# Optimization experiments

Measured on AMD Instinct MI355X. Metric: run time of the kernel, lower is better.

## Reference

```python
import jax, jax.numpy as jnp
import numpy as np

M = 4
L_LIST = [5, 7, 9, 11]
C = 256
GC = C // M  # group channels = 64
BN_EPS = 1e-5


def setup_inputs() -> dict:
    key = jax.random.key(0)
    ks = jax.random.split(key, 12)
    B, H, W = 4, 128, 128
    x = jax.random.normal(ks[0], (B, C, H, W), dtype=jnp.float32)
    # per-group 1x1 conv weights (no bias), stacked since same shape
    qw = jax.random.normal(ks[1], (M, GC, GC), dtype=jnp.float32) * 0.05
    kw = jax.random.normal(ks[2], (M, GC, GC), dtype=jnp.float32) * 0.05
    r_q = jax.random.normal(ks[3], (1, C, 1, 1), dtype=jnp.float32)
    rk0 = jax.random.normal(ks[4], (1, GC, 2 * L_LIST[0] - 1, 1, 1), dtype=jnp.float32)
    rk1 = jax.random.normal(ks[5], (1, GC, 2 * L_LIST[1] - 1, 1, 1), dtype=jnp.float32)
    rk2 = jax.random.normal(ks[6], (1, GC, 2 * L_LIST[2] - 1, 1, 1), dtype=jnp.float32)
    rk3 = jax.random.normal(ks[7], (1, GC, 2 * L_LIST[3] - 1, 1, 1), dtype=jnp.float32)
    fusion_w = jax.random.normal(ks[8], (C, C), dtype=jnp.float32) * 0.05
    bn_gamma = jnp.ones((C,), dtype=jnp.float32)
    bn_beta = jnp.zeros((C,), dtype=jnp.float32)
    return {"x": x, "qw": qw, "kw": kw, "r_q": r_q, "rk0": rk0, "rk1": rk1,
            "rk2": rk2, "rk3": rk3, "fusion_w": fusion_w,
            "bn_gamma": bn_gamma, "bn_beta": bn_beta}


def _axial(k, L):
    """Gather the cross-shaped (axial) neighborhood of size 2L-1 per pixel.

    Matches F.unfold(k, (L,L), padding=pad) followed by slicing the center
    column (vertical neighbors) and center row minus the center element
    (horizontal neighbors), in the original ordering:
      [k_h (L vertical), k_w_pre (pad left), k_w_post (L-pad-1 right)].
    Returns [B, gc, 2L-1, H, W] with zero padding at borders.
    """
    pad = (L - 1) // 2
    B, gc, H, W = k.shape
    kv = jnp.pad(k, ((0, 0), (0, 0), (pad, pad), (0, 0)))
    kh = jnp.pad(k, ((0, 0), (0, 0), (0, 0), (pad, pad)))
    parts = [kv[:, :, r:r + H, :] for r in range(L)]            # vertical offsets -pad..pad
    parts += [kh[:, :, :, r:r + W] for r in range(pad)]          # horizontal -pad..-1
    parts += [kh[:, :, :, r:r + W] for r in range(pad + 1, L)]   # horizontal +1..+pad
    return jnp.stack(parts, axis=2)


def reference(x, qw, kw, r_q, rk0, rk1, rk2, rk3, fusion_w, bn_gamma, bn_beta):
    rks = [rk0, rk1, rk2, rk3]
    B, Cc, H, W = x.shape
    qx = r_q + x
    outs = []
    for i, L in enumerate(L_LIST):
        xg = x[:, i * GC:(i + 1) * GC]
        qg = qx[:, i * GC:(i + 1) * GC]
        q = jnp.einsum('oc,bchw->bohw', qw[i], qg)   # 1x1 conv, no bias
        k = jnp.einsum('oc,bchw->bohw', kw[i], xg)
        ka = _axial(k, L) + rks[i]                   # [B, gc, 2L-1, H, W]
        # energy over channels then summed over the 2L-1 axial positions
        e = jnp.einsum('bchw,bcrhw->bhw', q, ka)
        outs.append(jnp.broadcast_to(e[:, None], (B, GC, H, W)))
    att = jnp.concatenate(outs, axis=1)              # [B, C, H, W]
    att = jnp.einsum('oc,bchw->bohw', fusion_w, att)
    # BatchNorm2d in training mode: batch statistics over (B, H, W)
    mean = att.mean(axis=(0, 2, 3))
    var = att.var(axis=(0, 2, 3))
    att = (att - mean[:, None, None]) * jax.lax.rsqrt(var[:, None, None] + BN_EPS)
    att = att * bn_gamma[:, None, None] + bn_beta[:, None, None]
    att = jax.nn.sigmoid(jax.nn.relu(att))
    return x * att
```

## Files before the change

### kernel.cpp

```cpp
#include <hip/hip_runtime.h>

#define Bb 4
#define Cc 256
#define GC_ 64
#define Hh 128
#define Wd 128
#define HWn 16384
#define NPIX 65536
#define EPS 1e-5f

#define T_OFF   0
#define E_OFF   16777216
#define ST_OFF  (E_OFF + NPIX*4)
#define A_OFF   (ST_OFF + 16)
#define CV_OFF  (A_OFF + 16384)
#define FW_OFF  (CV_OFF + 256)

typedef __attribute__((ext_vector_type(8))) short short8v;
typedef __attribute__((ext_vector_type(4))) float f32x4;
typedef unsigned short u16;

__device__ inline u16 f2bf(float f) {
    union { float f; unsigned u; } v; v.f = f;
    unsigned r = v.u + 0x7fff + ((v.u >> 16) & 1);
    return (u16)(r >> 16);
}
__device__ inline float bf2f(u16 u) {
    union { unsigned u; float f; } v; v.u = ((unsigned)u) << 16;
    return v.f;
}

__global__ __launch_bounds__(256) void k0_precompute(
    const float* __restrict__ qw, const float* __restrict__ kw,
    const float* __restrict__ rk0, const float* __restrict__ rk1,
    const float* __restrict__ rk2, const float* __restrict__ rk3,
    const float* __restrict__ fusion_w,
    u16* __restrict__ Abf, float* __restrict__ cvec, float* __restrict__ fwred,
    float* __restrict__ stats)
{
    const int tid = threadIdx.x;
    if (blockIdx.x == 4) {
        if (tid < 16) stats[tid] = 0.f;
        for (int i = 0; i < 4; ++i) {
            float s = 0.f;
            const float* fp = fusion_w + tid*256 + i*64;
            #pragma unroll 8
            for (int c = 0; c < 64; ++c) s += fp[c];
            fwred[tid*4 + i] = s;
        }
        return;
    }
    const int g = blockIdx.x;
    __shared__ float qwL[4096];
    __shared__ float kwL[4096];
    __shared__ float rks[64];
    for (int i = tid; i < 4096; i += 256) {
        qwL[i] = qw[g*4096 + i];
        kwL[i] = kw[g*4096 + i];
    }
    __syncthreads();
    if (tid < 64) {
        const float* rkp = (g==0)?rk0:(g==1)?rk1:(g==2)?rk2:rk3;
        const int R = 4*g + 9;
        float s = 0.f;
        for (int r = 0; r < R; ++r) s += rkp[tid*R + r];
        rks[tid] = s;
    }
    __syncthreads();
    for (int idx = tid; idx < 4096; idx += 256) {
        const int ct = idx >> 10, kh = (idx >> 9) & 1;
        const int lane = (idx >> 3) & 63, j = idx & 7;
        const int c = ct*16 + (lane & 15);
        const int d = kh*32 + (lane >> 4)*8 + j;
        float s = 0.f;
        #pragma unroll
        for (int o = 0; o < 64; ++o) s += qwL[o*64 + c] * kwL[o*64 + d];
        Abf[g*4096 + idx] = f2bf(s);
    }
    if (tid < 64) {
        float s = 0.f;
        #pragma unroll
        for (int o = 0; o < 64; ++o) s += qwL[o*64 + tid] * rks[o];
        cvec[g*64 + tid] = s;
    }
}

__global__ __launch_bounds__(256) void k1_mfma(
    const float* __restrict__ x, const u16* __restrict__ Abf,
    u16* __restrict__ t, u16* __restrict__ xbf)
{
    __shared__ u16 xt[64*132];
    const int tid = threadIdx.x;
    const int wv = tid >> 6, lane = tid & 63;
    const int chunk = blockIdx.x & 127;
    const int g = (blockIdx.x >> 7) & 3;
    const int b = blockIdx.x >> 9;
    const int l15 = lane & 15, lg = lane >> 4;
    const int px0 = chunk*128;

    const u16* Ab = Abf + g*4096;
    short8v afr[4][2];
    #pragma unroll
    for (int ct = 0; ct < 4; ++ct)
      #pragma unroll
      for (int kh = 0; kh < 2; ++kh)
        afr[ct][kh] = *(const short8v*)(Ab + ((ct*2 + kh)*64 + lane)*8);

    const float* xg = x   + (size_t)(b*Cc + g*GC_)*HWn;
    u16* tg        = t    + (size_t)(b*Cc + g*GC_)*HWn;
    u16* xbg       = xbf  + (size_t)(b*Cc + g*GC_)*HWn;

    #pragma unroll
    for (int i = 0; i < 8; ++i) {
        const int idx = tid + i*256;
        const int ch = idx >> 5, q = (idx & 31) << 2;
        const float4 v = *(const float4*)(xg + (size_t)ch*HWn + px0 + q);
        u16 o4[4] __attribute__((aligned(8))) = {f2bf(v.x), f2bf(v.y), f2bf(v.z), f2bf(v.w)};
        *(uint2*)(xt + ch*132 + q) = *(const uint2*)o4;
        *(uint2*)(xbg + (size_t)ch*HWn + px0 + q) = *(const uint2*)o4;
    }
    __syncthreads();

    const int pw = wv*32;
    #pragma unroll
    for (int nt = 0; nt < 2; ++nt) {
        const int pt = pw + nt*16 + l15;
        short8v bfr[2];
        #pragma unroll
        for (int kh = 0; kh < 2; ++kh)
          #pragma unroll
          for (int j = 0; j < 8; ++j)
            bfr[kh][j] = (short)xt[(kh*32 + lg*8 + j)*132 + pt];
        #pragma unroll
        for (int ct = 0; ct < 4; ++ct) {
            f32x4 acc = {0.f, 0.f, 0.f, 0.f};
            acc = __builtin_amdgcn_mfma_f32_16x16x32_bf16(bfr[0], afr[ct][0], acc, 0, 0, 0);
            acc = __builtin_amdgcn_mfma_f32_16x16x32_bf16(bfr[1], afr[ct][1], acc, 0, 0, 0);
            u16 ov[4] __attribute__((aligned(8)));
            #pragma unroll
            for (int r = 0; r < 4; ++r) ov[r] = f2bf(acc[r]);
            *(uint2*)(tg + (size_t)(ct*16 + l15)*HWn + px0 + pw + nt*16 + lg*4) = *(const uint2*)ov;
        }
    }
}

__global__ __launch_bounds__(256) void k23_fused(
    const u16* __restrict__ t, const u16* __restrict__ xbf,
    const float* __restrict__ r_q, const float* __restrict__ cvec,
    u16* __restrict__ eh)
{
    __shared__ u16 timg[4][18*132];
    __shared__ u16 simg[2][8*132];
    __shared__ float rqL[16], cvL[16];
    const int tid = threadIdx.x;
    const int bid = blockIdx.x;
    const int wk = (bid & 7)*128 + (bid >> 3);
    const int qh = wk & 3;
    const int htile = (wk >> 2) & 15;
    const int g = (wk >> 6) & 3;
    const int b = wk >> 8;
    const int p = g + 2;
    const int h0 = htile*8;
    const int c0 = qh*16;

    if (tid < 16) { rqL[tid] = r_q[g*64 + c0 + tid]; cvL[tid] = cvec[g*64 + c0 + tid]; }

    const u16* tbase = t   + (size_t)(b*Cc + g*GC_ + c0)*HWn;
    const u16* xbase = xbf + (size_t)(b*Cc + g*GC_ + c0)*HWn;

    #pragma unroll
    for (int k = 0; k < 3; ++k) {
        const int idx = tid + k*256;
        if (idx < 576) {
            const int r = idx >> 5, w4 = (idx & 31) << 2;
            const int hh = h0 - p + r;
            uint2 v0 = make_uint2(0u,0u), v1 = make_uint2(0u,0u);
            if (hh >= 0 && hh < 128) {
                v0 = *(const uint2*)(tbase + (hh<<7) + w4);
                v1 = *(const uint2*)(tbase + HWn + (hh<<7) + w4);
            }
            *(uint2*)(&timg[0][r*132 + w4]) = v0;
            *(uint2*)(&timg[1][r*132 + w4]) = v1;
        }
    }
    __syncthreads();

    const int vch = tid >> 7, vcol = tid & 127;
    const int hch = tid >> 7, hr = (tid & 127) >> 4, hseg = tid & 15, hw0 = hseg*8;
    float er[8];
    #pragma unroll
    for (int j = 0; j < 8; ++j) er[j] = 0.f;

    for (int it = 0; it < 8; ++it) {
        const int curp = (it & 1)*2;
        uint2 pr0[3], pr1[3];
        if (it < 7) {
            const u16* tn0 = tbase + (size_t)(2*it + 2)*HWn;
            const u16* tn1 = tn0 + HWn;
            #pragma unroll
            for (int k = 0; k < 3; ++k) {
                const int idx = tid + k*256;
                pr0[k] = make_uint2(0u,0u); pr1[k] = make_uint2(0u,0u);
                if (idx < 576) {
                    const int r = idx >> 5, w4 = (idx & 31) << 2;
                    const int hh = h0 - p + r;
                    if (hh >= 0 && hh < 128) {
                        pr0[k] = *(const uint2*)(tn0 + (hh<<7) + w4);
                        pr1[k] = *(const uint2*)(tn1 + (hh<<7) + w4);
                    }
                }
            }
        }

        {
            const u16* tb = &timg[curp + vch][0];
            float run = 0.f;
            for (int j = 0; j <= 2*p; ++j) run += bf2f(tb[j*132 + vcol]);
            #pragma unroll
            for (int i = 0; i < 8; ++i) {
                simg[vch][i*132 + vcol] = f2bf(run);
                if (i != 7)
                    run += bf2f(tb[(i + 1 + 2*p)*132 + vcol]) - bf2f(tb[i*132 + vcol]);
            }
        }
        __syncthreads();

        {
            const int cc = it*2 + hch;
            const u16* trow = &timg[curp + hch][(hr + p)*132];
            float run = 0.f;
            const int lo = max(hw0 - p, 0), hi = min(hw0 + p, 127);
            for (int ww = lo; ww <= hi; ++ww) run += bf2f(trow[ww]);
            const float rq = rqL[cc], cv = cvL[cc];
            union { uint4 q; u16 s[8]; } xu;
            xu.q = *(const uint4*)(xbase + (size_t)cc*HWn + ((h0 + hr) << 7) + hw0);
            #pragma unroll
            for (int j = 0; j < 8; ++j) {
                const int w = hw0 + j;
                const float S = run + bf2f(simg[hch][hr*132 + w]) - bf2f(trow[w]);
                er[j] += (bf2f(xu.s[j]) + rq) * (S + cv);
                run += (w + 1 + p < 128 ? bf2f(trow[w + 1 + p]) : 0.f)
                     - (w - p     >= 0  ? bf2f(trow[w - p])     : 0.f);
            }
        }
        if (it < 7) {
            const int nxt = curp ^ 2;
            #pragma unroll
            for (int k = 0; k < 3; ++k) {
                const int idx = tid + k*256;
                if (idx < 576) {
                    const int r = idx >> 5, w4 = (idx & 31) << 2;
                    *(uint2*)(&timg[nxt + 0][r*132 + w4]) = pr0[k];
                    *(uint2*)(&timg[nxt + 1][r*132 + w4]) = pr1[k];
                }
            }
        }
        __syncthreads();
    }

    u16 ov[8] __attribute__((aligned(16)));
    #pragma unroll
    for (int j = 0; j < 8; ++j) ov[j] = f2bf(er[j]);
    u16* ep = eh + (size_t)((qh*2 + hch)*16 + b*4 + g)*HWn + ((h0 + hr) << 7) + hw0;
    *(uint4*)ep = *(const uint4*)ov;
}

__global__ __launch_bounds__(256) void k3b_stats(
    const u16* __restrict__ eh, float* __restrict__ ebuf, float* __restrict__ stats)
{
    __shared__ float red[4*14];
    const int tid = threadIdx.x;
    const int q = blockIdx.x*256 + tid;
    const int b = q >> 14, p = q & (HWn - 1);
    float e4[4];
    #pragma unroll
    for (int g = 0; g < 4; ++g) {
        float s = 0.f;
        #pragma unroll
        for (int qq = 0; qq < 8; ++qq)
            s += bf2f(eh[(size_t)(qq*16 + b*4 + g)*HWn + p]);
        e4[g] = s;
        ebuf[(size_t)(b*4 + g)*HWn + p] = s;
    }
    const float e0 = e4[0], e1 = e4[1], e2 = e4[2], e3 = e4[3];
    float v[14];
    v[0]=e0; v[1]=e1; v[2]=e2; v[3]=e3;
    v[4]=e0*e0; v[5]=e0*e1; v[6]=e0*e2; v[7]=e0*e3;
    v[8]=e1*e1; v[9]=e1*e2; v[10]=e1*e3;
    v[11]=e2*e2; v[12]=e2*e3; v[13]=e3*e3;
    #pragma unroll
    for (int kk = 0; kk < 14; ++kk) {
        float s = v[kk];
        for (int off = 32; off > 0; off >>= 1) s += __shfl_down(s, off, 64);
        v[kk] = s;
    }
    const int lane = tid & 63, wv = tid >> 6;
    if (lane == 0) {
        #pragma unroll
        for (int kk = 0; kk < 14; ++kk) red[wv*14 + kk] = v[kk];
    }
    __syncthreads();
    if (tid < 14) atomicAdd(&stats[tid], red[tid] + red[14+tid] + red[28+tid] + red[42+tid]);
}

__global__ __launch_bounds__(256) void k5_out(
    const u16* __restrict__ xbf, const float* __restrict__ ebuf,
    const float* __restrict__ fwred, const float* __restrict__ stats,
    const float* __restrict__ gamma, const float* __restrict__ beta,
    float* __restrict__ out)
{
    const int tid = threadIdx.x;
    const int chunk = blockIdx.x & 15;
    const int oct = (blockIdx.x >> 4) & 31;
    const int b = blockIdx.x >> 9;
    __shared__ float alL[8], beL[8];
    __shared__ float4 fwL[8];
    if (tid < 8) {
        const int o = oct*8 + tid;
        const float invN = 1.f / (float)NPIX;
        const float me0 = stats[0]*invN, me1 = stats[1]*invN, me2 = stats[2]*invN, me3 = stats[3]*invN;
        const float m00 = stats[4]*invN,  m01 = stats[5]*invN,  m02 = stats[6]*invN,  m03 = stats[7]*invN;
        const float m11 = stats[8]*invN,  m12 = stats[9]*invN,  m13 = stats[10]*invN;
        const float m22 = stats[11]*invN, m23 = stats[12]*invN, m33 = stats[13]*invN;
        const float4 fw = ((const float4*)fwred)[o];
        const float Ef = fw.x*me0 + fw.y*me1 + fw.z*me2 + fw.w*me3;
        const float E2 = fw.x*fw.x*m00 + fw.y*fw.y*m11 + fw.z*fw.z*m22 + fw.w*fw.w*m33
                       + 2.f*(fw.x*fw.y*m01 + fw.x*fw.z*m02 + fw.x*fw.w*m03
                            + fw.y*fw.z*m12 + fw.y*fw.w*m13 + fw.z*fw.w*m23);
        const float a = gamma[o] * rsqrtf(E2 - Ef*Ef + EPS);
        alL[tid] = a;
        beL[tid] = beta[o] - Ef*a;
        fwL[tid] = fw;
    }
    __syncthreads();

    const int p0 = chunk*1024 + tid*4;
    const float* eb = ebuf + (size_t)b*4*HWn;
    const float4 E0 = *(const float4*)(eb + 0*HWn + p0);
    const float4 E1 = *(const float4*)(eb + 1*HWn + p0);
    const float4 E2v = *(const float4*)(eb + 2*HWn + p0);
    const float4 E3 = *(const float4*)(eb + 3*HWn + p0);

    #pragma unroll
    for (int c = 0; c < 8; ++c) {
        const int o = oct*8 + c;
        const float4 fw = fwL[c];
        const float al = alL[c], be = beL[c];
        float f[4];
        f[0] = fw.x*E0.x + fw.y*E1.x + fw.z*E2v.x + fw.w*E3.x;
        f[1] = fw.x*E0.y + fw.y*E1.y + fw.z*E2v.y + fw.w*E3.y;
        f[2] = fw.x*E0.z + fw.y*E1.z + fw.z*E2v.z + fw.w*E3.z;
        f[3] = fw.x*E0.w + fw.y*E1.w + fw.z*E2v.w + fw.w*E3.w;
        const size_t base = (size_t)(b*Cc + o)*HWn + p0;
        const uint2 xu = *(const uint2*)(xbf + base);
        float xa[4];
        xa[0] = bf2f((u16)(xu.x & 0xffff)); xa[1] = bf2f((u16)(xu.x >> 16));
        xa[2] = bf2f((u16)(xu.y & 0xffff)); xa[3] = bf2f((u16)(xu.y >> 16));
        float4 r; float* rp = &r.x;
        #pragma unroll
        for (int j = 0; j < 4; ++j) {
            float z = al*f[j] + be;
            z = fmaxf(z, 0.f);
            rp[j] = xa[j] / (1.f + __expf(-z));
        }
        *(float4*)(out + base) = r;
    }
}

extern "C" void kernel_launch(void* const* d_in, const int* in_sizes, int n_in,
                              void* d_out, int out_size, void* d_ws, size_t ws_size,
                              hipStream_t stream)
{
    const float* x   = (const float*)d_in[0];
    const float* qw  = (const float*)d_in[1];
    const float* kw  = (const float*)d_in[2];
    const float* r_q = (const float*)d_in[3];
    const float* rk0 = (const float*)d_in[4];
    const float* rk1 = (const float*)d_in[5];
    const float* rk2 = (const float*)d_in[6];
    const float* rk3 = (const float*)d_in[7];
    const float* fw  = (const float*)d_in[8];
    const float* gm  = (const float*)d_in[9];
    const float* bt  = (const float*)d_in[10];
    float* out = (float*)d_out;
    float* ws  = (float*)d_ws;

    u16*   t     = (u16*)(ws + T_OFF);
    u16*   xbf   = (u16*)ws + 16777216;
    float* ebuf  = ws + E_OFF;
    float* stats = ws + ST_OFF;
    u16*   Abf   = (u16*)(ws + A_OFF);
    float* cvec  = ws + CV_OFF;
    float* fwr   = ws + FW_OFF;
    u16*   eh    = (u16*)out;

    k0_precompute<<<5,    256, 0, stream>>>(qw, kw, rk0, rk1, rk2, rk3, fw, Abf, cvec, fwr, stats);
    k1_mfma      <<<2048, 256, 0, stream>>>(x, Abf, t, xbf);
    k23_fused    <<<1024, 256, 0, stream>>>(t, xbf, r_q, cvec, eh);
    k3b_stats    <<<256,  256, 0, stream>>>(eh, ebuf, stats);
    k5_out       <<<2048, 256, 0, stream>>>(xbf, ebuf, fwr, stats, gm, bt, out);
}
```

Measured before the change: 88.61 us.

## Give each wavefront its own LDS tile in k1 to drop block barrier

The k1 projection kernel now has each wavefront stage its own 64-pixel, 64-channel slice of x into a private LDS region and run the MFMA on it. This removes the block-wide __syncthreads. Each block now covers 256 pixels instead of 128, so the grid is halved to 1024 blocks. Each wave issues 16 loads and 4 MFMA tiles, which gives more independent work per wave but less parallelism across blocks. Global read coalescing drops to 256-byte segments per channel row.

```diff
diff --git a/kernel.cpp b/kernel.cpp
--- a/kernel.cpp
+++ b/kernel.cpp
@@ -89,14 +89,14 @@
     const float* __restrict__ x, const u16* __restrict__ Abf,
     u16* __restrict__ t, u16* __restrict__ xbf)
 {
-    __shared__ u16 xt[64*132];
+    __shared__ u16 xt[4][64*68];
     const int tid = threadIdx.x;
     const int wv = tid >> 6, lane = tid & 63;
-    const int chunk = blockIdx.x & 127;
-    const int g = (blockIdx.x >> 7) & 3;
-    const int b = blockIdx.x >> 9;
+    const int chunk = blockIdx.x & 63;
+    const int g = (blockIdx.x >> 6) & 3;
+    const int b = blockIdx.x >> 8;
     const int l15 = lane & 15, lg = lane >> 4;
-    const int px0 = chunk*128;
+    const int px0w = chunk*256 + wv*64;
 
     const u16* Ab = Abf + g*4096;
     short8v afr[4][2];
@@ -109,28 +109,29 @@
     const float* xg = x   + (size_t)(b*Cc + g*GC_)*HWn;
     u16* tg        = t    + (size_t)(b*Cc + g*GC_)*HWn;
     u16* xbg       = xbf  + (size_t)(b*Cc + g*GC_)*HWn;
-
-    #pragma unroll
-    for (int i = 0; i < 8; ++i) {
-        const int idx = tid + i*256;
-        const int ch = idx >> 5, q = (idx & 31) << 2;
-        const float4 v = *(const float4*)(xg + (size_t)ch*HWn + px0 + q);
+    u16* xw = &xt[wv][0];
+
+    const int pxo = l15 << 2;
+    #pragma unroll
+    for (int i = 0; i < 16; ++i) {
+        const int ch = i*4 + lg;
+        const float4 v = *(const float4*)(xg + (size_t)ch*HWn + px0w + pxo);
         u16 o4[4] __attribute__((aligned(8))) = {f2bf(v.x), f2bf(v.y), f2bf(v.z), f2bf(v.w)};
-        *(uint2*)(xt + ch*132 + q) = *(const uint2*)o4;
-        *(uint2*)(xbg + (size_t)ch*HWn + px0 + q) = *(const uint2*)o4;
-    }
-    __syncthreads();
-
-    const int pw = wv*32;
+        *(uint2*)(xw + ch*68 + pxo) = *(const uint2*)o4;
+        *(uint2*)(xbg + (size_t)ch*HWn + px0w + pxo) = *(const uint2*)o4;
+    }
+
     #pragma unroll
     for (int nt = 0; nt < 2; ++nt) {
-        const int pt = pw + nt*16 + l15;
+        const int pt = nt*32 + ((lane & 1) << 4) + l15;
+        (void)pt;
+        const int px = nt*16 + l15;
         short8v bfr[2];
         #pragma unroll
         for (int kh = 0; kh < 2; ++kh)
           #pragma unroll
           for (int j = 0; j < 8; ++j)
-            bfr[kh][j] = (short)xt[(kh*32 + lg*8 + j)*132 + pt];
+            bfr[kh][j] = (short)xw[(kh*32 + lg*8 + j)*68 + px];
         #pragma unroll
         for (int ct = 0; ct < 4; ++ct) {
             f32x4 acc = {0.f, 0.f, 0.f, 0.f};
@@ -139,7 +140,27 @@
             u16 ov[4] __attribute__((aligned(8)));
             #pragma unroll
             for (int r = 0; r < 4; ++r) ov[r] = f2bf(acc[r]);
-            *(uint2*)(tg + (size_t)(ct*16 + l15)*HWn + px0 + pw + nt*16 + lg*4) = *(const uint2*)ov;
+            *(uint2*)(tg + (size_t)(ct*16 + l15)*HWn + px0w + nt*16 + lg*4) = *(const uint2*)ov;
+        }
+    }
+    #pragma unroll
+    for (int nt = 2; nt < 4; ++nt) {
+        const int px = nt*16 + l15;
+        short8v bfr[2];
+        #pragma unroll
+        for (int kh = 0; kh < 2; ++kh)
+          #pragma unroll
+          for (int j = 0; j < 8; ++j)
+            bfr[kh][j] = (short)xw[(kh*32 + lg*8 + j)*68 + px];
+        #pragma unroll
+        for (int ct = 0; ct < 4; ++ct) {
+            f32x4 acc = {0.f, 0.f, 0.f, 0.f};
+            acc = __builtin_amdgcn_mfma_f32_16x16x32_bf16(bfr[0], afr[ct][0], acc, 0, 0, 0);
+            acc = __builtin_amdgcn_mfma_f32_16x16x32_bf16(bfr[1], afr[ct][1], acc, 0, 0, 0);
+            u16 ov[4] __attribute__((aligned(8)));
+            #pragma unroll
+            for (int r = 0; r < 4; ++r) ov[r] = f2bf(acc[r]);
+            *(uint2*)(tg + (size_t)(ct*16 + l15)*HWn + px0w + nt*16 + lg*4) = *(const uint2*)ov;
         }
     }
 }
@@ -395,7 +416,7 @@
     u16*   eh    = (u16*)out;
 
     k0_precompute<<<5,    256, 0, stream>>>(qw, kw, rk0, rk1, rk2, rk3, fw, Abf, cvec, fwr, stats);
-    k1_mfma      <<<2048, 256, 0, stream>>>(x, Abf, t, xbf);
+    k1_mfma      <<<1024, 256, 0, stream>>>(x, Abf, t, xbf);
     k23_fused    <<<1024, 256, 0, stream>>>(t, xbf, r_q, cvec, eh);
     k3b_stats    <<<256,  256, 0, stream>>>(eh, ebuf, stats);
     k5_out       <<<2048, 256, 0, stream>>>(xbf, ebuf, fwr, stats, gm, bt, out);
```

Result: no change. 89.63 us (+1.1%).
